# Performance work log

Measured on AMD Instinct MI355X. Metric: run time of the kernel, lower is better.

The kernel has to match this reference:

```python
import jax, jax.numpy as jnp
import numpy as np

B, S, D = 4, 4096, 1024
H, HID, ATT = 16, 64, 64


def setup_inputs() -> dict:
    key = jax.random.key(0)
    ks = jax.random.split(key, 7)
    sc = 0.02
    return {
        "x": jax.random.normal(ks[0], (B, S, D), dtype=jnp.float32),
        "Wq": jax.random.normal(ks[1], (D, H * HID), dtype=jnp.float32) * sc,
        "bq": jnp.zeros((H * HID,), dtype=jnp.float32),
        "Wk": jax.random.normal(ks[2], (D, H * HID), dtype=jnp.float32) * sc,
        "bk": jnp.zeros((H * HID,), dtype=jnp.float32),
        "Wv": jax.random.normal(ks[3], (D, H * ATT), dtype=jnp.float32) * sc,
        "bv": jnp.zeros((H * ATT,), dtype=jnp.float32),
    }


def reference(x, Wq, bq, Wk, bk, Wv, bv):
    b, s, _ = x.shape
    q = (x @ Wq + bq).reshape(b, s, H, HID)
    k = (x @ Wk + bk).reshape(b, s, H, HID)
    v = (x @ Wv + bv).reshape(b, s, H, ATT)
    # attention across the head axis: [B,S,H,H] scores per token
    scores = jnp.einsum("bsid,bsjd->bsij", q, k) / np.sqrt(HID).astype(np.float32)
    probs = jax.nn.softmax(scores, axis=-1)
    ctx = jnp.einsum("bsij,bsja->bsia", probs, v)
    return ctx.reshape(b, s, H * ATT)
```

## Files before the change

kernel.cpp:

```cpp
#include <hip/hip_runtime.h>


#define AS1 __attribute__((address_space(1)))
#define AS3 __attribute__((address_space(3)))

typedef __bf16 bf16x8 __attribute__((ext_vector_type(8)));
typedef float f32x4 __attribute__((ext_vector_type(4)));
typedef unsigned short u16x8 __attribute__((ext_vector_type(8)));

static constexpr int MTOK = 16384;
static constexpr int N3   = 3072;
static constexpr int KD   = 1024;
static constexpr int BK   = 32;
static constexpr int NT   = KD / BK;

__device__ __forceinline__ unsigned short f2bf(float f) {
  unsigned u = __float_as_uint(f);
  unsigned r = u + 0x7FFFu + ((u >> 16) & 1u);
  return (unsigned short)(r >> 16);
}
__device__ __forceinline__ float bf2f(unsigned short s) {
  return __uint_as_float(((unsigned)s) << 16);
}

__device__ __forceinline__ void gload_lds16(const void* g, void* lds_uniform) {
  __builtin_amdgcn_global_load_lds((const AS1 void*)g, (AS3 void*)lds_uniform, 16, 0, 0);
}

__global__ __launch_bounds__(256) void cvt_x_kernel(const float* __restrict__ x,
                                                    unsigned short* __restrict__ xb) {
  int i = blockIdx.x * 256 + threadIdx.x;
  const float4* p = (const float4*)x;
  float4 a = p[2 * i], b = p[2 * i + 1];
  u16x8 o;
  o[0] = f2bf(a.x); o[1] = f2bf(a.y); o[2] = f2bf(a.z); o[3] = f2bf(a.w);
  o[4] = f2bf(b.x); o[5] = f2bf(b.y); o[6] = f2bf(b.z); o[7] = f2bf(b.w);
  *((u16x8*)xb + i) = o;
}

__global__ __launch_bounds__(256) void prep_w_kernel(const float* __restrict__ Wq,
                                                     const float* __restrict__ Wk,
                                                     const float* __restrict__ Wv,
                                                     const float* __restrict__ bq,
                                                     const float* __restrict__ bk,
                                                     const float* __restrict__ bv,
                                                     unsigned short* __restrict__ WT,
                                                     float* __restrict__ bcat) {
  __shared__ float tile[32][33];
  int kt = blockIdx.x * 32;
  int nt = blockIdx.y * 32;
  const float* W; const float* bias; int nb;
  if (nt < 1024)      { W = Wq; bias = bq; nb = nt; }
  else if (nt < 2048) { W = Wk; bias = bk; nb = nt - 1024; }
  else                { W = Wv; bias = bv; nb = nt - 2048; }
  int tx = threadIdx.x & 31, ty = threadIdx.x >> 5;
#pragma unroll
  for (int it = 0; it < 4; ++it) {
    int kk = it * 8 + ty;
    tile[kk][tx] = W[(size_t)(kt + kk) * 1024 + nb + tx];
  }
  __syncthreads();
#pragma unroll
  for (int it = 0; it < 4; ++it) {
    int nn = it * 8 + ty;
    WT[(size_t)(nt + nn) * 1024 + kt + tx] = f2bf(tile[tx][nn]);
  }
  if (blockIdx.x == 0 && threadIdx.x < 32)
    bcat[nt + threadIdx.x] = bias[nb + threadIdx.x];
}

__global__ __launch_bounds__(512, 2) void gemm_qkv_kernel(const unsigned short* __restrict__ A,
                                                          const unsigned short* __restrict__ Bt,
                                                          const float* __restrict__ bias,
                                                          unsigned short* __restrict__ C) {
  __shared__ __align__(16) unsigned short lds[4][16384];
  const int tid  = threadIdx.x;
  const int lane = tid & 63;
  const int wave = tid >> 6;
  const int wm = wave >> 2, wn = wave & 3;
  const int m0 = blockIdx.x * 256;
  const int n0 = blockIdx.y * 256;
  const int chunk = lane >> 4;
  const int hl = lane & 15;

  const int srow = tid >> 2;
  const int sp   = tid & 3;
  const int gc_lo = (sp ^ ((srow >> 1) & 3)) * 8;
  const size_t arow0 = (size_t)(m0 + srow) * KD;
  const size_t arow1 = (size_t)(m0 + 128 + srow) * KD;
  const size_t brow0 = (size_t)(n0 + srow) * KD;
  const size_t brow1 = (size_t)(n0 + 128 + srow) * KD;
  const int ubase = wave * 512;

  int aoff[8], boff[4];
#pragma unroll
  for (int m = 0; m < 8; ++m) {
    int row = wm * 128 + m * 16 + hl;
    aoff[m] = row * 32 + (chunk ^ ((row >> 1) & 3)) * 8;
  }
#pragma unroll
  for (int n = 0; n < 4; ++n) {
    int row = wn * 64 + n * 16 + hl;
    boff[n] = 8192 + row * 32 + (chunk ^ ((row >> 1) & 3)) * 8;
  }

  f32x4 acc[8][4] = {};

#define STAGE(T)                                                                 \
  do {                                                                           \
    unsigned short* buf = lds[(T) & 3];                                          \
    int kt = (T) * BK;                                                           \
    gload_lds16(A  + arow0 + kt + gc_lo, buf + ubase);                           \
    gload_lds16(A  + arow1 + kt + gc_lo, buf + 4096 + ubase);                    \
    gload_lds16(Bt + brow0 + kt + gc_lo, buf + 8192 + ubase);                    \
    gload_lds16(Bt + brow1 + kt + gc_lo, buf + 12288 + ubase);                   \
  } while (0)

#define COMPUTE(T)                                                               \
  do {                                                                           \
    const unsigned short* buf = lds[(T) & 3];                                    \
    bf16x8 af[8], bfr[4];                                                        \
    _Pragma("unroll") for (int m = 0; m < 8; ++m)                                \
      af[m] = *(const bf16x8*)&buf[aoff[m]];                                     \
    _Pragma("unroll") for (int n = 0; n < 4; ++n)                                \
      bfr[n] = *(const bf16x8*)&buf[boff[n]];                                    \
    _Pragma("unroll") for (int m = 0; m < 8; ++m)                                \
      _Pragma("unroll") for (int n = 0; n < 4; ++n)                              \
        acc[m][n] = __builtin_amdgcn_mfma_f32_16x16x32_bf16(af[m], bfr[n],       \
                                                            acc[m][n], 0, 0, 0); \
  } while (0)

  STAGE(0); STAGE(1); STAGE(2);

  for (int t = 0; t < NT - 3; ++t) {
    STAGE(t + 3);
    asm volatile("s_waitcnt vmcnt(12)\n\ts_barrier" ::: "memory");
    COMPUTE(t);
    asm volatile("s_barrier" ::: "memory");
  }
  asm volatile("s_waitcnt vmcnt(8)\n\ts_barrier" ::: "memory");
  COMPUTE(NT - 3);
  asm volatile("s_barrier" ::: "memory");
  asm volatile("s_waitcnt vmcnt(4)\n\ts_barrier" ::: "memory");
  COMPUTE(NT - 2);
  asm volatile("s_barrier" ::: "memory");
  asm volatile("s_waitcnt vmcnt(0)\n\ts_barrier" ::: "memory");
  COMPUTE(NT - 1);
#undef STAGE
#undef COMPUTE

#pragma unroll
  for (int n = 0; n < 4; ++n) {
    int col = n0 + wn * 64 + n * 16 + hl;
    float bv = bias[col];
#pragma unroll
    for (int m = 0; m < 8; ++m) {
      int rowb = m0 + wm * 128 + m * 16 + chunk * 4;
#pragma unroll
      for (int r = 0; r < 4; ++r) {
        float v = acc[m][n][r] + bv;
        C[(size_t)(rowb + r) * N3 + col] = f2bf(v);
      }
    }
  }
}

__global__ __launch_bounds__(256) void attn_kernel(const unsigned short* __restrict__ qkv,
                                                   float* __restrict__ out) {
  __shared__ float p_lds[4][16][17];
  const int tid = threadIdx.x;
  const int lane = tid & 63;
  const int w = tid >> 6;
  const size_t token = (size_t)blockIdx.x * 4 + w;
  const unsigned short* rowp = qkv + token * N3;
  const int head = lane & 15;
  const int chunk = lane >> 4;

  const int o = head * 64 + chunk * 8;
  bf16x8 q0 = *(const bf16x8*)(rowp + o);
  bf16x8 q1 = *(const bf16x8*)(rowp + o + 32);
  bf16x8 k0 = *(const bf16x8*)(rowp + 1024 + o);
  bf16x8 k1 = *(const bf16x8*)(rowp + 1024 + o + 32);
  f32x4 c = {0.f, 0.f, 0.f, 0.f};
  c = __builtin_amdgcn_mfma_f32_16x16x32_bf16(q0, k0, c, 0, 0, 0);
  c = __builtin_amdgcn_mfma_f32_16x16x32_bf16(q1, k1, c, 0, 0, 0);

#pragma unroll
  for (int r = 0; r < 4; ++r) {
    float s = c[r] * 0.125f;
    float m = s;
#pragma unroll
    for (int off = 1; off < 16; off <<= 1) m = fmaxf(m, __shfl_xor(m, off, 64));
    float e = __expf(s - m);
    float sum = e;
#pragma unroll
    for (int off = 1; off < 16; off <<= 1) sum += __shfl_xor(sum, off, 64);
    p_lds[w][chunk * 4 + r][head] = e / sum;
  }
  __syncthreads();

  const int i = lane >> 2;
  const int ab = lane & 3;
  const unsigned short* vbase = rowp + 2048 + ab * 16;
  float accv[16];
#pragma unroll
  for (int cc = 0; cc < 16; ++cc) accv[cc] = 0.f;
#pragma unroll
  for (int j = 0; j < 16; ++j) {
    float pij = p_lds[w][i][j];
    u16x8 v0 = *(const u16x8*)(vbase + j * 64);
    u16x8 v1 = *(const u16x8*)(vbase + j * 64 + 8);
#pragma unroll
    for (int cc = 0; cc < 8; ++cc) accv[cc] += pij * bf2f(v0[cc]);
#pragma unroll
    for (int cc = 0; cc < 8; ++cc) accv[8 + cc] += pij * bf2f(v1[cc]);
  }
  float* op = out + token * 1024 + i * 64 + ab * 16;
#pragma unroll
  for (int cc = 0; cc < 16; cc += 4) {
    f32x4 v = {accv[cc], accv[cc + 1], accv[cc + 2], accv[cc + 3]};
    *(f32x4*)(op + cc) = v;
  }
}

extern "C" void kernel_launch(void* const* d_in, const int* in_sizes, int n_in,
                              void* d_out, int out_size, void* d_ws, size_t ws_size,
                              hipStream_t stream) {
  const float* x  = (const float*)d_in[0];
  const float* Wq = (const float*)d_in[1];
  const float* bq = (const float*)d_in[2];
  const float* Wk = (const float*)d_in[3];
  const float* bk = (const float*)d_in[4];
  const float* Wv = (const float*)d_in[5];
  const float* bv = (const float*)d_in[6];
  float* out = (float*)d_out;

  char* ws = (char*)d_ws;
  unsigned short* xb   = (unsigned short*)ws;
  unsigned short* WT   = (unsigned short*)(ws + 33554432);
  float*          bcat = (float*)(ws + 39845888);
  unsigned short* qkv  = (unsigned short*)(ws + 39858176);

  cvt_x_kernel<<<dim3((MTOK * KD / 8) / 256), 256, 0, stream>>>(x, xb);
  prep_w_kernel<<<dim3(32, 96), 256, 0, stream>>>(Wq, Wk, Wv, bq, bk, bv, WT, bcat);
  gemm_qkv_kernel<<<dim3(MTOK / 256, N3 / 256), 512, 0, stream>>>(xb, WT, bcat, qkv);
  attn_kernel<<<dim3(MTOK / 4), 256, 0, stream>>>(qkv, out);
}
```

Before: 178.4 us.

## Restructure QKV GEMM main loop to issue prefetch after LDS reads with priority boost

Rewrites the GEMM K-loop so each phase first reads its fragments from LDS, then issues the global-to-LDS prefetch into the slot just freed, then barriers and runs the MFMAs under raised wave priority. This replaces the old stage-then-wait-then-compute loop that needed two barriers per step, and unrolls four slots per iteration with constant LDS offsets. It aims to overlap global loads with MFMA work and cut barrier and address overhead. The slot reuse depends on a correct barrier order, so a mistake here could cause LDS races.

```diff
diff --git a/kernel.cpp b/kernel.cpp
--- a/kernel.cpp
+++ b/kernel.cpp
@@ -11,8 +11,6 @@
 static constexpr int MTOK = 16384;
 static constexpr int N3   = 3072;
 static constexpr int KD   = 1024;
-static constexpr int BK   = 32;
-static constexpr int NT   = KD / BK;
 
 __device__ __forceinline__ unsigned short f2bf(float f) {
   unsigned u = __float_as_uint(f);
@@ -73,7 +71,7 @@
                                                           const unsigned short* __restrict__ Bt,
                                                           const float* __restrict__ bias,
                                                           unsigned short* __restrict__ C) {
-  __shared__ __align__(16) unsigned short lds[4][16384];
+  __shared__ __align__(16) unsigned short lds[65536];
   const int tid  = threadIdx.x;
   const int lane = tid & 63;
   const int wave = tid >> 6;
@@ -84,13 +82,11 @@
   const int hl = lane & 15;
 
   const int srow = tid >> 2;
-  const int sp   = tid & 3;
-  const int gc_lo = (sp ^ ((srow >> 1) & 3)) * 8;
-  const size_t arow0 = (size_t)(m0 + srow) * KD;
-  const size_t arow1 = (size_t)(m0 + 128 + srow) * KD;
-  const size_t brow0 = (size_t)(n0 + srow) * KD;
-  const size_t brow1 = (size_t)(n0 + 128 + srow) * KD;
-  const int ubase = wave * 512;
+  const int sc   = ((tid & 3) ^ ((srow >> 1) & 3)) * 8;
+  const size_t asrc0 = (size_t)(m0 + srow) * KD + sc;
+  const size_t asrc1 = (size_t)(m0 + 128 + srow) * KD + sc;
+  const size_t bsrc0 = (size_t)(n0 + srow) * KD + sc;
+  const size_t bsrc1 = (size_t)(n0 + 128 + srow) * KD + sc;
 
   int aoff[8], boff[4];
 #pragma unroll
@@ -106,60 +102,70 @@
 
   f32x4 acc[8][4] = {};
 
-#define STAGE(T)                                                                 \
-  do {                                                                           \
-    unsigned short* buf = lds[(T) & 3];                                          \
-    int kt = (T) * BK;                                                           \
-    gload_lds16(A  + arow0 + kt + gc_lo, buf + ubase);                           \
-    gload_lds16(A  + arow1 + kt + gc_lo, buf + 4096 + ubase);                    \
-    gload_lds16(Bt + brow0 + kt + gc_lo, buf + 8192 + ubase);                    \
-    gload_lds16(Bt + brow1 + kt + gc_lo, buf + 12288 + ubase);                   \
+#define STAGE(SLOT, KK)                                                        \
+  do {                                                                         \
+    unsigned short* dst = lds + (SLOT) * 16384 + tid * 8;                      \
+    gload_lds16(A  + asrc0 + (KK), dst);                                       \
+    gload_lds16(A  + asrc1 + (KK), dst + 4096);                                \
+    gload_lds16(Bt + bsrc0 + (KK), dst + 8192);                                \
+    gload_lds16(Bt + bsrc1 + (KK), dst + 12288);                               \
   } while (0)
 
-#define COMPUTE(T)                                                               \
-  do {                                                                           \
-    const unsigned short* buf = lds[(T) & 3];                                    \
-    bf16x8 af[8], bfr[4];                                                        \
-    _Pragma("unroll") for (int m = 0; m < 8; ++m)                                \
-      af[m] = *(const bf16x8*)&buf[aoff[m]];                                     \
-    _Pragma("unroll") for (int n = 0; n < 4; ++n)                                \
-      bfr[n] = *(const bf16x8*)&buf[boff[n]];                                    \
-    _Pragma("unroll") for (int m = 0; m < 8; ++m)                                \
-      _Pragma("unroll") for (int n = 0; n < 4; ++n)                              \
-        acc[m][n] = __builtin_amdgcn_mfma_f32_16x16x32_bf16(af[m], bfr[n],       \
-                                                            acc[m][n], 0, 0, 0); \
+#define PH(SLOT, DOSTAGE, STSLOT, KREAD)                                       \
+  do {                                                                         \
+    const unsigned short* bufp = lds + (SLOT) * 16384;                         \
+    bf16x8 af[8], bfr[4];                                                      \
+    _Pragma("unroll") for (int m = 0; m < 8; ++m)                              \
+      af[m] = *(const bf16x8*)(bufp + aoff[m]);                                \
+    _Pragma("unroll") for (int n = 0; n < 4; ++n)                              \
+      bfr[n] = *(const bf16x8*)(bufp + boff[n]);                               \
+    if (DOSTAGE) { STAGE(STSLOT, (KREAD) + 96); }                              \
+    __builtin_amdgcn_s_barrier();                             \
+    asm volatile("s_waitcnt lgkmcnt(0)" ::: "memory");                         \
+    __builtin_amdgcn_sched_barrier(0);                                         \
+    __builtin_amdgcn_s_setprio(1);                                             \
+    _Pragma("unroll") for (int m = 0; m < 8; ++m)                              \
+      _Pragma("unroll") for (int n = 0; n < 4; ++n)                            \
+        acc[m][n] = __builtin_amdgcn_mfma_f32_16x16x32_bf16(af[m], bfr[n],     \
+                                                            acc[m][n], 0, 0, 0);\
+    __builtin_amdgcn_s_setprio(0);                                             \
   } while (0)
 
-  STAGE(0); STAGE(1); STAGE(2);
-
-  for (int t = 0; t < NT - 3; ++t) {
-    STAGE(t + 3);
-    asm volatile("s_waitcnt vmcnt(12)\n\ts_barrier" ::: "memory");
-    COMPUTE(t);
-    asm volatile("s_barrier" ::: "memory");
-  }
-  asm volatile("s_waitcnt vmcnt(8)\n\ts_barrier" ::: "memory");
-  COMPUTE(NT - 3);
-  asm volatile("s_barrier" ::: "memory");
-  asm volatile("s_waitcnt vmcnt(4)\n\ts_barrier" ::: "memory");
-  COMPUTE(NT - 2);
-  asm volatile("s_barrier" ::: "memory");
-  asm volatile("s_waitcnt vmcnt(0)\n\ts_barrier" ::: "memory");
-  COMPUTE(NT - 1);
+#define SYNC(VM)                                                               \
+  do {                                                                         \
+    asm volatile("s_waitcnt vmcnt(" #VM ")" ::: "memory");                     \
+    __builtin_amdgcn_s_barrier();                             \
+    __builtin_amdgcn_sched_barrier(0);                                         \
+  } while (0)
+
+  STAGE(0, 0); STAGE(1, 32); STAGE(2, 64);
+
+#pragma unroll 1
+  for (int t = 0; t < 7; ++t) {
+    const int kb = t * 128;
+    SYNC(8); PH(0, true, 3, kb);
+    SYNC(8); PH(1, true, 0, kb + 32);
+    SYNC(8); PH(2, true, 1, kb + 64);
+    SYNC(8); PH(3, true, 2, kb + 96);
+  }
+  SYNC(8); PH(0, true, 3, 896);
+  SYNC(8); PH(1, false, 0, 928);
+  SYNC(4); PH(2, false, 0, 960);
+  SYNC(0); PH(3, false, 0, 992);
 #undef STAGE
-#undef COMPUTE
+#undef PH
+#undef SYNC
 
 #pragma unroll
   for (int n = 0; n < 4; ++n) {
     int col = n0 + wn * 64 + n * 16 + hl;
-    float bv = bias[col];
+    float bvv = bias[col];
 #pragma unroll
     for (int m = 0; m < 8; ++m) {
       int rowb = m0 + wm * 128 + m * 16 + chunk * 4;
 #pragma unroll
       for (int r = 0; r < 4; ++r) {
-        float v = acc[m][n][r] + bv;
-        C[(size_t)(rowb + r) * N3 + col] = f2bf(v);
+        C[(size_t)(rowb + r) * N3 + col] = f2bf(acc[m][n][r] + bvv);
       }
     }
   }
```

Measured after the change: 175.3 us. No clear change (-1.7%).
